# Kernel optimization log

Measured on AMD Instinct MI355X. Metric: run time of the kernel, lower is better.

Reference implementation:

```python
import jax, jax.numpy as jnp
import numpy as np

N_USERS = 100000  # n_users + 1 (padding idx)
N_ITEMS = 100000  # n_items + 1
N_NODES = N_USERS + N_ITEMS
EMBED = 64
N_BEHAVIORS = 3
N_EDGES = 2000000
BATCH = 4096
REG_WEIGHT = 1e-4


def setup_inputs() -> dict:
    key = jax.random.key(0)
    ks = jax.random.split(key, 6)
    user_emb = jax.random.normal(ks[0], (N_USERS, EMBED), dtype=jnp.float32) * 0.05
    item_emb = jax.random.normal(ks[1], (N_ITEMS, EMBED), dtype=jnp.float32) * 0.05
    gcn_weight = jax.random.normal(ks[2], (N_BEHAVIORS, EMBED, EMBED), dtype=jnp.float32) * (1.0 / np.sqrt(EMBED))
    gcn_bias = jnp.zeros((N_BEHAVIORS, EMBED), dtype=jnp.float32)
    edges = jax.random.randint(ks[3], (N_BEHAVIORS, 2, N_EDGES), 0, N_NODES, dtype=jnp.int64)
    batch_data = jax.random.randint(ks[4], (BATCH, N_BEHAVIORS, 3), 0, N_USERS, dtype=jnp.int64)
    return {"user_emb": user_emb, "item_emb": item_emb, "gcn_weight": gcn_weight,
            "gcn_bias": gcn_bias, "edges": edges, "batch_data": batch_data}


def _gcn_conv(x, row, col, W, b):
    # PyG GCNConv, add_self_loops=False: out = D^-1/2 A D^-1/2 (x W) + b
    x = x @ W  # [N, d]
    deg = jax.ops.segment_sum(jnp.ones_like(col, dtype=x.dtype), col, num_segments=N_NODES)
    dinv = jnp.where(deg > 0, jax.lax.rsqrt(jnp.maximum(deg, 1.0)) * (deg > 0), 0.0)
    norm = dinv[row] * dinv[col]  # [E]
    msg = norm[:, None] * x[row]  # [E, d] gather + scale
    out = jax.ops.segment_sum(msg, col, num_segments=N_NODES)  # scatter-add
    return out + b


def _l2_normalize(x, eps=1e-12):
    n = jnp.sqrt(jnp.sum(x * x, axis=-1, keepdims=True))
    return x / jnp.maximum(n, eps)


def reference(user_emb, item_emb, gcn_weight, gcn_bias, edges, batch_data):
    total = jnp.concatenate([user_emb, item_emb], axis=0)  # [N_NODES, d]
    total_loss = jnp.float32(0.0)
    for bi in range(N_BEHAVIORS):
        row, col = edges[bi, 0], edges[bi, 1]
        layer = _gcn_conv(total, row, col, gcn_weight[bi], gcn_bias[bi])
        layer = _l2_normalize(layer)
        total = layer + total  # residual accumulation across behaviors
        u_all, i_all = total[:N_USERS], total[N_USERS:]
        users = batch_data[:, bi, 0]          # [B]
        items = batch_data[:, bi, 1:]         # [B, 2] (pos, neg)
        u_feat = u_all[users]                 # [B, d]
        i_feat = i_all[items]                 # [B, 2, d]
        scores = jnp.einsum('bd,bkd->bk', u_feat, i_feat)  # [B, 2]
        bpr = -jnp.mean(jax.nn.log_sigmoid(scores[:, 0] - scores[:, 1]))
        total_loss = total_loss + bpr
    emb_loss = 0.5 * (jnp.sum(user_emb * user_emb) + jnp.sum(item_emb * item_emb)) / BATCH
    total_loss = total_loss + REG_WEIGHT * emb_loss
    return total_loss
```

## Files before the change

### kernel.cpp

```cpp
#include <hip/hip_runtime.h>

#define N_USERS  100000
#define N_ITEMS  100000
#define N_NODES  200000
#define EMBED    64
#define NB       3
#define N_EDGESC 2000000
#define NE_TOT   (NB * N_EDGESC)
#define BATCH    4096
#define M_SEG    (NB * N_NODES)
#define NPART    500
#define PSIZE    400
#define NBUCK    (NB * NPART)
#define NBLKB    256
#define EPB      8192
#define STAGE_CAP 4416
#define GEMM_BLOCKS 3125
#define AGG_BLOCKS 6250
#define NPARTS   (GEMM_BLOCKS + NB * 1024)

typedef unsigned short u16;
typedef __attribute__((ext_vector_type(8))) short short8;
typedef __attribute__((ext_vector_type(4))) float f32x4;

__device__ __forceinline__ float b2f(u16 h) {
    return __uint_as_float(((unsigned)h) << 16);
}
__device__ __forceinline__ u16 f2b(float f) {
    unsigned u = __float_as_uint(f);
    return (u16)((u + 0x7FFF + ((u >> 16) & 1)) >> 16);
}

__global__ __launch_bounds__(256) void scatterA(const int* __restrict__ edges,
                                                int* __restrict__ H) {
    __shared__ int h[NPART];
    int bi  = blockIdx.x / NBLKB;
    int blk = blockIdx.x - bi * NBLKB;
    const int* cols = edges + ((size_t)bi * 2 + 1) * N_EDGESC;
    for (int i = threadIdx.x; i < NPART; i += 256) h[i] = 0;
    __syncthreads();
    int base0 = blk * EPB;
#pragma unroll 4
    for (int it = 0; it < EPB / 256; ++it) {
        int idx = base0 + it * 256 + threadIdx.x;
        if (idx < N_EDGESC) atomicAdd(&h[cols[idx] / PSIZE], 1);
    }
    __syncthreads();
    for (int i = threadIdx.x; i < NPART; i += 256)
        H[(bi * NPART + i) * NBLKB + blk] = h[i];
}

__global__ __launch_bounds__(256) void colscan(int* __restrict__ H,
                                               int* __restrict__ bCnt) {
    int wid = blockIdx.x * 4 + (threadIdx.x >> 6);
    if (wid >= NBUCK) return;
    int lane = threadIdx.x & 63;
    int carry = 0;
#pragma unroll
    for (int ch = 0; ch < NBLKB / 64; ++ch) {
        int i = wid * NBLKB + ch * 64 + lane;
        int v = H[i];
        int s = v;
#pragma unroll
        for (int off = 1; off < 64; off <<= 1) {
            int tt = __shfl_up(s, off, 64);
            if (lane >= off) s += tt;
        }
        H[i] = carry + s - v;
        carry += __shfl(s, 63, 64);
    }
    if (lane == 0) bCnt[wid] = carry;
}

__global__ __launch_bounds__(256) void scan_buckets(const int* __restrict__ bCnt,
                                                    int* __restrict__ bBase,
                                                    int* __restrict__ startv) {
    __shared__ int s[NBUCK + 1];
    __shared__ int tsum[256];
    int t = threadIdx.x;
    const int IT = (NBUCK + 255) / 256;
    int base0 = t * IT;
    int vals[IT];
    int sum = 0;
#pragma unroll
    for (int k = 0; k < IT; ++k) {
        int i = base0 + k;
        vals[k] = (i < NBUCK) ? bCnt[i] : 0;
        sum += vals[k];
    }
    tsum[t] = sum;
    __syncthreads();
    for (int off = 1; off < 256; off <<= 1) {
        int v = (t >= off) ? tsum[t - off] : 0;
        __syncthreads();
        tsum[t] += v;
        __syncthreads();
    }
    int run = tsum[t] - sum;
#pragma unroll
    for (int k = 0; k < IT; ++k) {
        int i = base0 + k;
        if (i < NBUCK) s[i] = run;
        run += vals[k];
    }
    if (t == 255) {
        s[NBUCK] = run;
        startv[M_SEG] = run;
    }
    __syncthreads();
    for (int i = t; i < NBUCK + 1; i += 256) bBase[i] = s[i];
}

__global__ __launch_bounds__(256) void scatterB(const int* __restrict__ edges,
                                                const int* __restrict__ H,
                                                const int* __restrict__ bCnt,
                                                const int* __restrict__ bBase,
                                                int* __restrict__ bpack) {
    __shared__ int cur[NPART + 2];
    __shared__ int lstart[NPART + 1];
    __shared__ int sbase[NPART];
    __shared__ int tsum[256];
    __shared__ int stage[EPB];
    int bi  = blockIdx.x / NBLKB;
    int blk = blockIdx.x - bi * NBLKB;
    const int* rows = edges + ((size_t)bi * 2 + 0) * N_EDGESC;
    const int* cols = edges + ((size_t)bi * 2 + 1) * N_EDGESC;
    int t = threadIdx.x;

    for (int i = t; i < NPART; i += 256) {
        int b  = bi * NPART + i;
        int hc = H[b * NBLKB + blk];
        int nx = (blk < NBLKB - 1) ? H[b * NBLKB + blk + 1] : bCnt[b];
        sbase[i] = bBase[b] + hc;
        cur[i]   = nx - hc;
    }
    if (t == 0) cur[NPART] = 0;
    __syncthreads();

    int sb0 = t * 2;
    int v0 = (sb0     <= NPART) ? cur[sb0]     : 0;
    int v1 = (sb0 + 1 <= NPART) ? cur[sb0 + 1] : 0;
    int sum = v0 + v1;
    tsum[t] = sum;
    __syncthreads();
    for (int off = 1; off < 256; off <<= 1) {
        int v = (t >= off) ? tsum[t - off] : 0;
        __syncthreads();
        tsum[t] += v;
        __syncthreads();
    }
    int run = tsum[t] - sum;
    __syncthreads();
    if (sb0     <= NPART) { cur[sb0]     = run;      lstart[sb0]     = run; }
    if (sb0 + 1 <= NPART) { cur[sb0 + 1] = run + v0; lstart[sb0 + 1] = run + v0; }
    __syncthreads();

    int base0 = blk * EPB;
    for (int it = 0; it < EPB / 256; it += 4) {
        int i0 = base0 + (it + 0) * 256 + t;
        int i1 = base0 + (it + 1) * 256 + t;
        int i2 = base0 + (it + 2) * 256 + t;
        int i3 = base0 + (it + 3) * 256 + t;
        int c0 = (i0 < N_EDGESC) ? cols[i0] : -1;
        int c1 = (i1 < N_EDGESC) ? cols[i1] : -1;
        int c2 = (i2 < N_EDGESC) ? cols[i2] : -1;
        int c3 = (i3 < N_EDGESC) ? cols[i3] : -1;
        int r0 = (i0 < N_EDGESC) ? rows[i0] : 0;
        int r1 = (i1 < N_EDGESC) ? rows[i1] : 0;
        int r2 = (i2 < N_EDGESC) ? rows[i2] : 0;
        int r3 = (i3 < N_EDGESC) ? rows[i3] : 0;
        if (c0 >= 0) { int p = c0 / PSIZE; int q = atomicAdd(&cur[p], 1);
                       stage[q] = ((c0 - p * PSIZE) << 18) | r0; }
        if (c1 >= 0) { int p = c1 / PSIZE; int q = atomicAdd(&cur[p], 1);
                       stage[q] = ((c1 - p * PSIZE) << 18) | r1; }
        if (c2 >= 0) { int p = c2 / PSIZE; int q = atomicAdd(&cur[p], 1);
                       stage[q] = ((c2 - p * PSIZE) << 18) | r2; }
        if (c3 >= 0) { int p = c3 / PSIZE; int q = atomicAdd(&cur[p], 1);
                       stage[q] = ((c3 - p * PSIZE) << 18) | r3; }
    }
    __syncthreads();

    int grp = t >> 4;
    int li  = t & 15;
    for (int p = grp; p < NPART; p += 16) {
        int lb  = lstart[p];
        int len = lstart[p + 1] - lb;
        int gb  = sbase[p];
        for (int off = li; off < len; off += 16)
            bpack[gb + off] = stage[lb + off];
    }
}

__global__ __launch_bounds__(256) void place_kernel(const int* __restrict__ bpack,
                                                    const int* __restrict__ bBase,
                                                    int* __restrict__ startv,
                                                    float* __restrict__ dinv,
                                                    int* __restrict__ srow) {
    __shared__ int cnt[PSIZE + 2];
    __shared__ int tsum[256];
    __shared__ int stage[STAGE_CAP];
    int b    = blockIdx.x;
    int bi   = b / NPART;
    int part = b - bi * NPART;
    int segBase = bi * N_NODES + part * PSIZE;
    int lo = bBase[b], hiEnd = bBase[b + 1];
    int t = threadIdx.x;

    for (int i = t; i < PSIZE + 1; i += 256) cnt[i] = 0;
    __syncthreads();

    {
        int i = lo + t;
        for (; i + 768 < hiEnd; i += 1024) {
            int a0 = bpack[i];
            int a1 = bpack[i + 256];
            int a2 = bpack[i + 512];
            int a3 = bpack[i + 768];
            atomicAdd(&cnt[a0 >> 18], 1);
            atomicAdd(&cnt[a1 >> 18], 1);
            atomicAdd(&cnt[a2 >> 18], 1);
            atomicAdd(&cnt[a3 >> 18], 1);
        }
        for (; i < hiEnd; i += 256) atomicAdd(&cnt[bpack[i] >> 18], 1);
    }
    __syncthreads();

    int base0 = t * 2;
    int v0 = (base0     <= PSIZE) ? cnt[base0]     : 0;
    int v1 = (base0 + 1 <= PSIZE) ? cnt[base0 + 1] : 0;
    int sum = v0 + v1;
    tsum[t] = sum;
    __syncthreads();
    for (int off = 1; off < 256; off <<= 1) {
        int v = (t >= off) ? tsum[t - off] : 0;
        __syncthreads();
        tsum[t] += v;
        __syncthreads();
    }
    int run = tsum[t] - sum;
    __syncthreads();
    if (base0     <= PSIZE) cnt[base0]     = run;
    if (base0 + 1 <= PSIZE) cnt[base0 + 1] = run + v0;
    __syncthreads();

    for (int i = t; i < PSIZE; i += 256) {
        int excl = cnt[i];
        int d    = cnt[i + 1] - excl;
        startv[segBase + i] = lo + excl;
        dinv[segBase + i]   = (d > 0) ? rsqrtf((float)d) : 0.0f;
    }
    __syncthreads();

    {
        int i = lo + t;
        for (; i + 768 < hiEnd; i += 1024) {
            int p0 = bpack[i];
            int p1 = bpack[i + 256];
            int p2 = bpack[i + 512];
            int p3 = bpack[i + 768];
            int q0 = atomicAdd(&cnt[p0 >> 18], 1);
            int q1 = atomicAdd(&cnt[p1 >> 18], 1);
            int q2 = atomicAdd(&cnt[p2 >> 18], 1);
            int q3 = atomicAdd(&cnt[p3 >> 18], 1);
            if (q0 < STAGE_CAP) stage[q0] = p0 & 0x3FFFF; else srow[lo + q0] = p0 & 0x3FFFF;
            if (q1 < STAGE_CAP) stage[q1] = p1 & 0x3FFFF; else srow[lo + q1] = p1 & 0x3FFFF;
            if (q2 < STAGE_CAP) stage[q2] = p2 & 0x3FFFF; else srow[lo + q2] = p2 & 0x3FFFF;
            if (q3 < STAGE_CAP) stage[q3] = p3 & 0x3FFFF; else srow[lo + q3] = p3 & 0x3FFFF;
        }
        for (; i < hiEnd; i += 256) {
            int pk  = bpack[i];
            int pos = atomicAdd(&cnt[pk >> 18], 1);
            if (pos < STAGE_CAP) stage[pos] = pk & 0x3FFFF; else srow[lo + pos] = pk & 0x3FFFF;
        }
    }
    __syncthreads();

    int n = hiEnd - lo;
    int cap = (n < STAGE_CAP) ? n : STAGE_CAP;
    for (int i = t; i < cap; i += 256) srow[lo + i] = stage[i];
}

__device__ __forceinline__ void load_Bfrag(const float* __restrict__ W,
                                           int lane, short8 Bf[4][2]) {
    int n    = lane & 15;
    int kb   = (lane >> 4) * 8;
#pragma unroll
    for (int ct = 0; ct < 4; ++ct)
#pragma unroll
        for (int kt = 0; kt < 2; ++kt)
#pragma unroll
            for (int j = 0; j < 8; ++j)
                Bf[ct][kt][j] = (short)f2b(W[(kt * 32 + kb + j) * 64 + ct * 16 + n]);
}

__device__ __forceinline__ void store_tile(u16* __restrict__ x16,
                                           const float* __restrict__ dinv, int base,
                                           int r0, int lane, const f32x4 acc[4]) {
    int col  = lane & 15;
    int rowb = (lane >> 4) * 4;
    float dv[4];
#pragma unroll
    for (int j = 0; j < 4; ++j) dv[j] = dinv[base + r0 + rowb + j];
#pragma unroll
    for (int ct = 0; ct < 4; ++ct)
#pragma unroll
        for (int j = 0; j < 4; ++j)
            x16[(size_t)(r0 + rowb + j) * 64 + ct * 16 + col] = f2b(acc[ct][j] * dv[j]);
}

__global__ __launch_bounds__(256) void mfma_first(const float* __restrict__ ue,
                                                  const float* __restrict__ ie,
                                                  const float* __restrict__ W,
                                                  const float* __restrict__ dinv,
                                                  u16* __restrict__ x16,
                                                  float* __restrict__ regpart) {
    __shared__ float wsum[4];
    int lane = threadIdx.x & 63;
    short8 Bf[4][2];
    load_Bfrag(W, lane, Bf);

    int r0 = (blockIdx.x * 4 + (threadIdx.x >> 6)) * 16;
    int m  = lane & 15;
    int kb = (lane >> 4) * 8;
    int r  = r0 + m;
    const float* src = (r < N_USERS) ? (ue + (size_t)r * 64)
                                     : (ie + (size_t)(r - N_USERS) * 64);
    float sq = 0.0f;
    short8 A0, A1;
#pragma unroll
    for (int h = 0; h < 2; ++h) {
        float4 a = ((const float4*)(src + h * 32 + kb))[0];
        float4 b = ((const float4*)(src + h * 32 + kb))[1];
        short8& A = h ? A1 : A0;
        A[0] = (short)f2b(a.x); A[1] = (short)f2b(a.y);
        A[2] = (short)f2b(a.z); A[3] = (short)f2b(a.w);
        A[4] = (short)f2b(b.x); A[5] = (short)f2b(b.y);
        A[6] = (short)f2b(b.z); A[7] = (short)f2b(b.w);
        sq += a.x * a.x + a.y * a.y + a.z * a.z + a.w * a.w;
        sq += b.x * b.x + b.y * b.y + b.z * b.z + b.w * b.w;
    }
    f32x4 acc[4];
#pragma unroll
    for (int ct = 0; ct < 4; ++ct) {
        acc[ct] = (f32x4){0.f, 0.f, 0.f, 0.f};
        acc[ct] = __builtin_amdgcn_mfma_f32_16x16x32_bf16(A0, Bf[ct][0], acc[ct], 0, 0, 0);
        acc[ct] = __builtin_amdgcn_mfma_f32_16x16x32_bf16(A1, Bf[ct][1], acc[ct], 0, 0, 0);
    }
    store_tile(x16, dinv, 0, r0, lane, acc);

#pragma unroll
    for (int off = 32; off; off >>= 1) sq += __shfl_xor(sq, off, 64);
    if (lane == 0) wsum[threadIdx.x >> 6] = sq;
    __syncthreads();
    if (threadIdx.x == 0)
        regpart[blockIdx.x] = (wsum[0] + wsum[1] + wsum[2] + wsum[3]) *
                              (0.5f * 0.0001f / (float)BATCH);
}

__global__ __launch_bounds__(256) void mfma_gemm(const u16* __restrict__ g16,
                                                 const float* __restrict__ W,
                                                 const float* __restrict__ dinv,
                                                 int base,
                                                 u16* __restrict__ x16) {
    int lane = threadIdx.x & 63;
    short8 Bf[4][2];
    load_Bfrag(W, lane, Bf);

    int r0 = (blockIdx.x * 4 + (threadIdx.x >> 6)) * 16;
    int m  = lane & 15;
    int kb = (lane >> 4) * 8;
    const u16* src = g16 + (size_t)(r0 + m) * 64 + kb;
    short8 A0 = *(const short8*)(src);
    short8 A1 = *(const short8*)(src + 32);
    f32x4 acc[4];
#pragma unroll
    for (int ct = 0; ct < 4; ++ct) {
        acc[ct] = (f32x4){0.f, 0.f, 0.f, 0.f};
        acc[ct] = __builtin_amdgcn_mfma_f32_16x16x32_bf16(A0, Bf[ct][0], acc[ct], 0, 0, 0);
        acc[ct] = __builtin_amdgcn_mfma_f32_16x16x32_bf16(A1, Bf[ct][1], acc[ct], 0, 0, 0);
    }
    store_tile(x16, dinv, base, r0, lane, acc);
}

__global__ __launch_bounds__(256) void agg_kernel(const int* __restrict__ srow,
                                                  const int* __restrict__ startv,
                                                  const float* __restrict__ dinv,
                                                  const int4* __restrict__ xv,
                                                  const float4* __restrict__ reslo,
                                                  const float4* __restrict__ reshi,
                                                  const int4* __restrict__ res16,
                                                  int resf32,
                                                  int4* __restrict__ g16out,
                                                  const float* __restrict__ bias,
                                                  int base ) {
    int lane = threadIdx.x & 63;
    int li   = lane & 7;
    int c = (blockIdx.x * 4 + (threadIdx.x >> 6)) * 8 + (lane >> 3);

    int   s   = startv[base + c];
    int   end = startv[base + c + 1];
    float dc  = dinv[base + c];

    float acc[8];
#pragma unroll
    for (int d = 0; d < 8; ++d) acc[d] = 0.0f;

    int e = s;
    for (; e + 8 <= end; e += 8) {
#pragma unroll
        for (int jj = 0; jj < 8; ++jj) {
            int r = srow[e + jj];
            int4 w = xv[(size_t)r * 8 + li];
            acc[0] += __uint_as_float(((unsigned)w.x) << 16);
            acc[1] += __uint_as_float(((unsigned)w.x) & 0xFFFF0000u);
            acc[2] += __uint_as_float(((unsigned)w.y) << 16);
            acc[3] += __uint_as_float(((unsigned)w.y) & 0xFFFF0000u);
            acc[4] += __uint_as_float(((unsigned)w.z) << 16);
            acc[5] += __uint_as_float(((unsigned)w.z) & 0xFFFF0000u);
            acc[6] += __uint_as_float(((unsigned)w.w) << 16);
            acc[7] += __uint_as_float(((unsigned)w.w) & 0xFFFF0000u);
        }
    }
    if (e < end) {
#pragma unroll
        for (int jj = 0; jj < 8; ++jj) {
            int  ej = e + jj;
            bool ok = ej < end;
            int  ec = ok ? ej : s;
            int  r  = srow[ec];
            int4 w  = xv[(size_t)r * 8 + li];
            float m = ok ? 1.0f : 0.0f;
            acc[0] += m * __uint_as_float(((unsigned)w.x) << 16);
            acc[1] += m * __uint_as_float(((unsigned)w.x) & 0xFFFF0000u);
            acc[2] += m * __uint_as_float(((unsigned)w.y) << 16);
            acc[3] += m * __uint_as_float(((unsigned)w.y) & 0xFFFF0000u);
            acc[4] += m * __uint_as_float(((unsigned)w.z) << 16);
            acc[5] += m * __uint_as_float(((unsigned)w.z) & 0xFFFF0000u);
            acc[6] += m * __uint_as_float(((unsigned)w.w) << 16);
            acc[7] += m * __uint_as_float(((unsigned)w.w) & 0xFFFF0000u);
        }
    }

    float4 b0 = ((const float4*)bias)[li * 2];
    float4 b1 = ((const float4*)bias)[li * 2 + 1];
    float v[8];
    v[0] = acc[0] * dc + b0.x; v[1] = acc[1] * dc + b0.y;
    v[2] = acc[2] * dc + b0.z; v[3] = acc[3] * dc + b0.w;
    v[4] = acc[4] * dc + b1.x; v[5] = acc[5] * dc + b1.y;
    v[6] = acc[6] * dc + b1.z; v[7] = acc[7] * dc + b1.w;
    float sq = 0.0f;
#pragma unroll
    for (int d = 0; d < 8; ++d) sq += v[d] * v[d];
    sq += __shfl_xor(sq, 1, 64);
    sq += __shfl_xor(sq, 2, 64);
    sq += __shfl_xor(sq, 4, 64);
    float inv = 1.0f / fmaxf(sqrtf(sq), 1e-12f);

    float rv[8];
    if (resf32) {
        const float4* rsrc = (c < N_USERS)
            ? reslo + ((size_t)c * 16 + li * 2)
            : reshi + ((size_t)(c - N_USERS) * 16 + li * 2);
        float4 t0 = rsrc[0], t1 = rsrc[1];
        rv[0] = t0.x; rv[1] = t0.y; rv[2] = t0.z; rv[3] = t0.w;
        rv[4] = t1.x; rv[5] = t1.y; rv[6] = t1.z; rv[7] = t1.w;
    } else {
        int4 rw = res16[(size_t)c * 8 + li];
        rv[0] = __uint_as_float(((unsigned)rw.x) << 16);
        rv[1] = __uint_as_float(((unsigned)rw.x) & 0xFFFF0000u);
        rv[2] = __uint_as_float(((unsigned)rw.y) << 16);
        rv[3] = __uint_as_float(((unsigned)rw.y) & 0xFFFF0000u);
        rv[4] = __uint_as_float(((unsigned)rw.z) << 16);
        rv[5] = __uint_as_float(((unsigned)rw.z) & 0xFFFF0000u);
        rv[6] = __uint_as_float(((unsigned)rw.w) << 16);
        rv[7] = __uint_as_float(((unsigned)rw.w) & 0xFFFF0000u);
    }
    float o[8];
#pragma unroll
    for (int d = 0; d < 8; ++d) o[d] = rv[d] + v[d] * inv;
    int4 h;
    h.x = (int)(((unsigned)f2b(o[0])) | (((unsigned)f2b(o[1])) << 16));
    h.y = (int)(((unsigned)f2b(o[2])) | (((unsigned)f2b(o[3])) << 16));
    h.z = (int)(((unsigned)f2b(o[4])) | (((unsigned)f2b(o[5])) << 16));
    h.w = (int)(((unsigned)f2b(o[6])) | (((unsigned)f2b(o[7])) << 16));
    g16out[(size_t)c * 8 + li] = h;
}

__global__ __launch_bounds__(256) void bpr_kernel(const u16* __restrict__ g16,
                                                  const int* __restrict__ batch,
                                                  int bi, float* __restrict__ bprpart) {
    __shared__ float sp4[4];
    int b    = blockIdx.x * 4 + (threadIdx.x >> 6);
    int lane = threadIdx.x & 63;
    int u  = batch[((size_t)b * NB + bi) * 3 + 0];
    int i0 = batch[((size_t)b * NB + bi) * 3 + 1];
    int i1 = batch[((size_t)b * NB + bi) * 3 + 2];
    float uf = b2f(g16[(size_t)u * 64 + lane]);
    float f0 = b2f(g16[(size_t)(N_USERS + i0) * 64 + lane]);
    float f1 = b2f(g16[(size_t)(N_USERS + i1) * 64 + lane]);
    float d  = uf * (f0 - f1);
#pragma unroll
    for (int off = 32; off; off >>= 1) d += __shfl_xor(d, off, 64);
    float sp = (d > 0.0f) ? log1pf(expf(-d)) : (-d + log1pf(expf(d)));
    if (lane == 0) sp4[threadIdx.x >> 6] = sp;
    __syncthreads();
    if (threadIdx.x == 0)
        bprpart[blockIdx.x] = (sp4[0] + sp4[1] + sp4[2] + sp4[3]) * (1.0f / BATCH);
}

__global__ __launch_bounds__(256) void final_write(const float* __restrict__ parts,
                                                   float* __restrict__ out) {
    __shared__ float ws[4];
    float s = 0.0f;
    for (int i = threadIdx.x; i < NPARTS; i += 256) s += parts[i];
#pragma unroll
    for (int off = 32; off; off >>= 1) s += __shfl_xor(s, off, 64);
    if ((threadIdx.x & 63) == 0) ws[threadIdx.x >> 6] = s;
    __syncthreads();
    if (threadIdx.x == 0) out[0] = ws[0] + ws[1] + ws[2] + ws[3];
}

extern "C" void kernel_launch(void* const* d_in, const int* in_sizes, int n_in,
                              void* d_out, int out_size, void* d_ws, size_t ws_size,
                              hipStream_t stream) {
    const float* user_emb = (const float*)d_in[0];
    const float* item_emb = (const float*)d_in[1];
    const float* gcn_w    = (const float*)d_in[2];
    const float* gcn_b    = (const float*)d_in[3];
    const int*   edges    = (const int*)d_in[4];
    const int*   batch    = (const int*)d_in[5];
    float*       out      = (float*)d_out;

    const size_t NODE_F = (size_t)N_NODES * EMBED;
    u16*     g16A   = (u16*)d_ws;
    u16*     g16B   = g16A + NODE_F;
    u16*     x16    = g16B + NODE_F;
    float*   dinv   = (float*)(x16 + NODE_F);
    int*     startv = (int*)(dinv + M_SEG);
    int*     Hglob  = startv + M_SEG + 1;
    int*     bCnt   = Hglob + NBUCK * NBLKB;
    int*     bBase  = bCnt + NBUCK;
    int*     bpack  = bBase + NBUCK + 1;
    int*     srow   = bpack + NE_TOT;
    float*   parts  = (float*)(srow + NE_TOT);
    float*   regpart = parts;
    float*   bprpart = parts + GEMM_BLOCKS;

    scatterA<<<NB * NBLKB, 256, 0, stream>>>(edges, Hglob);
    colscan<<<(NBUCK + 3) / 4, 256, 0, stream>>>(Hglob, bCnt);
    scan_buckets<<<1, 256, 0, stream>>>(bCnt, bBase, startv);
    scatterB<<<NB * NBLKB, 256, 0, stream>>>(edges, Hglob, bCnt, bBase, bpack);
    place_kernel<<<NBUCK, 256, 0, stream>>>(bpack, bBase, startv, dinv, srow);

    mfma_first<<<GEMM_BLOCKS, 256, 0, stream>>>(user_emb, item_emb,
                                                gcn_w, dinv, x16, regpart);

    agg_kernel<<<AGG_BLOCKS, 256, 0, stream>>>(
        srow, startv, dinv, (const int4*)x16,
        (const float4*)user_emb, (const float4*)item_emb,
        (const int4*)0, 1,
        (int4*)g16A, gcn_b, 0);
    bpr_kernel<<<1024, 256, 0, stream>>>(g16A, batch, 0, bprpart);

    u16* gcur = g16A;
    u16* gnxt = g16B;
    for (int bi = 1; bi < NB; ++bi) {
        mfma_gemm<<<GEMM_BLOCKS, 256, 0, stream>>>(
            gcur, gcn_w + (size_t)bi * EMBED * EMBED, dinv, bi * N_NODES, x16);
        agg_kernel<<<AGG_BLOCKS, 256, 0, stream>>>(
            srow, startv, dinv, (const int4*)x16,
            (const float4*)0, (const float4*)0,
            (const int4*)gcur, 0,
            (int4*)gnxt, gcn_b + bi * EMBED, bi * N_NODES);
        bpr_kernel<<<1024, 256, 0, stream>>>(gnxt, batch, bi, bprpart + bi * 1024);
        u16* tmp = gcur; gcur = gnxt; gnxt = tmp;
    }
    final_write<<<1, 256, 0, stream>>>(parts, out);
}
```

Measured before the change: 384.1 us.

## Assign one wavefront per destination node in aggregation, splitting edges across lane groups

```diff
diff --git a/kernel.cpp b/kernel.cpp
--- a/kernel.cpp
+++ b/kernel.cpp
@@ -16,7 +16,7 @@
 #define EPB      8192
 #define STAGE_CAP 4416
 #define GEMM_BLOCKS 3125
-#define AGG_BLOCKS 6250
+#define AGG_BLOCKS 50000
 #define NPARTS   (GEMM_BLOCKS + NB * 1024)
 
 typedef unsigned short u16;
@@ -395,7 +395,8 @@
                                                   int base ) {
     int lane = threadIdx.x & 63;
     int li   = lane & 7;
-    int c = (blockIdx.x * 4 + (threadIdx.x >> 6)) * 8 + (lane >> 3);
+    int eg   = lane >> 3;
+    int c = blockIdx.x * 4 + (threadIdx.x >> 6);
 
     int   s   = startv[base + c];
     int   end = startv[base + c + 1];
@@ -405,40 +406,42 @@
 #pragma unroll
     for (int d = 0; d < 8; ++d) acc[d] = 0.0f;
 
-    int e = s;
-    for (; e + 8 <= end; e += 8) {
-#pragma unroll
-        for (int jj = 0; jj < 8; ++jj) {
-            int r = srow[e + jj];
-            int4 w = xv[(size_t)r * 8 + li];
-            acc[0] += __uint_as_float(((unsigned)w.x) << 16);
-            acc[1] += __uint_as_float(((unsigned)w.x) & 0xFFFF0000u);
-            acc[2] += __uint_as_float(((unsigned)w.y) << 16);
-            acc[3] += __uint_as_float(((unsigned)w.y) & 0xFFFF0000u);
-            acc[4] += __uint_as_float(((unsigned)w.z) << 16);
-            acc[5] += __uint_as_float(((unsigned)w.z) & 0xFFFF0000u);
-            acc[6] += __uint_as_float(((unsigned)w.w) << 16);
-            acc[7] += __uint_as_float(((unsigned)w.w) & 0xFFFF0000u);
+    for (int e = s; e < end; e += 16) {
+        int  e0 = e + eg;
+        bool k0 = e0 < end;
+        int  r0 = srow[k0 ? e0 : s];
+        int4 w0 = xv[(size_t)r0 * 8 + li];
+        float m0 = k0 ? 1.0f : 0.0f;
+        acc[0] += m0 * __uint_as_float(((unsigned)w0.x) << 16);
+        acc[1] += m0 * __uint_as_float(((unsigned)w0.x) & 0xFFFF0000u);
+        acc[2] += m0 * __uint_as_float(((unsigned)w0.y) << 16);
+        acc[3] += m0 * __uint_as_float(((unsigned)w0.y) & 0xFFFF0000u);
+        acc[4] += m0 * __uint_as_float(((unsigned)w0.z) << 16);
+        acc[5] += m0 * __uint_as_float(((unsigned)w0.z) & 0xFFFF0000u);
+        acc[6] += m0 * __uint_as_float(((unsigned)w0.w) << 16);
+        acc[7] += m0 * __uint_as_float(((unsigned)w0.w) & 0xFFFF0000u);
+        if (e + 8 < end) {
+            int  e1 = e + 8 + eg;
+            bool k1 = e1 < end;
+            int  r1 = srow[k1 ? e1 : s];
+            int4 w1 = xv[(size_t)r1 * 8 + li];
+            float m1 = k1 ? 1.0f : 0.0f;
+            acc[0] += m1 * __uint_as_float(((unsigned)w1.x) << 16);
+            acc[1] += m1 * __uint_as_float(((unsigned)w1.x) & 0xFFFF0000u);
+            acc[2] += m1 * __uint_as_float(((unsigned)w1.y) << 16);
+            acc[3] += m1 * __uint_as_float(((unsigned)w1.y) & 0xFFFF0000u);
+            acc[4] += m1 * __uint_as_float(((unsigned)w1.z) << 16);
+            acc[5] += m1 * __uint_as_float(((unsigned)w1.z) & 0xFFFF0000u);
+            acc[6] += m1 * __uint_as_float(((unsigned)w1.w) << 16);
+            acc[7] += m1 * __uint_as_float(((unsigned)w1.w) & 0xFFFF0000u);
         }
     }
-    if (e < end) {
-#pragma unroll
-        for (int jj = 0; jj < 8; ++jj) {
-            int  ej = e + jj;
-            bool ok = ej < end;
-            int  ec = ok ? ej : s;
-            int  r  = srow[ec];
-            int4 w  = xv[(size_t)r * 8 + li];
-            float m = ok ? 1.0f : 0.0f;
-            acc[0] += m * __uint_as_float(((unsigned)w.x) << 16);
-            acc[1] += m * __uint_as_float(((unsigned)w.x) & 0xFFFF0000u);
-            acc[2] += m * __uint_as_float(((unsigned)w.y) << 16);
-            acc[3] += m * __uint_as_float(((unsigned)w.y) & 0xFFFF0000u);
-            acc[4] += m * __uint_as_float(((unsigned)w.z) << 16);
-            acc[5] += m * __uint_as_float(((unsigned)w.z) & 0xFFFF0000u);
-            acc[6] += m * __uint_as_float(((unsigned)w.w) << 16);
-            acc[7] += m * __uint_as_float(((unsigned)w.w) & 0xFFFF0000u);
-        }
+
+#pragma unroll
+    for (int d = 0; d < 8; ++d) {
+        acc[d] += __shfl_xor(acc[d], 8, 64);
+        acc[d] += __shfl_xor(acc[d], 16, 64);
+        acc[d] += __shfl_xor(acc[d], 32, 64);
     }
 
     float4 b0 = ((const float4*)bias)[li * 2];
@@ -456,34 +459,36 @@
     sq += __shfl_xor(sq, 4, 64);
     float inv = 1.0f / fmaxf(sqrtf(sq), 1e-12f);
 
-    float rv[8];
-    if (resf32) {
-        const float4* rsrc = (c < N_USERS)
-            ? reslo + ((size_t)c * 16 + li * 2)
-            : reshi + ((size_t)(c - N_USERS) * 16 + li * 2);
-        float4 t0 = rsrc[0], t1 = rsrc[1];
-        rv[0] = t0.x; rv[1] = t0.y; rv[2] = t0.z; rv[3] = t0.w;
-        rv[4] = t1.x; rv[5] = t1.y; rv[6] = t1.z; rv[7] = t1.w;
-    } else {
-        int4 rw = res16[(size_t)c * 8 + li];
-        rv[0] = __uint_as_float(((unsigned)rw.x) << 16);
-        rv[1] = __uint_as_float(((unsigned)rw.x) & 0xFFFF0000u);
-        rv[2] = __uint_as_float(((unsigned)rw.y) << 16);
-        rv[3] = __uint_as_float(((unsigned)rw.y) & 0xFFFF0000u);
-        rv[4] = __uint_as_float(((unsigned)rw.z) << 16);
-        rv[5] = __uint_as_float(((unsigned)rw.z) & 0xFFFF0000u);
-        rv[6] = __uint_as_float(((unsigned)rw.w) << 16);
-        rv[7] = __uint_as_float(((unsigned)rw.w) & 0xFFFF0000u);
-    }
-    float o[8];
-#pragma unroll
-    for (int d = 0; d < 8; ++d) o[d] = rv[d] + v[d] * inv;
-    int4 h;
-    h.x = (int)(((unsigned)f2b(o[0])) | (((unsigned)f2b(o[1])) << 16));
-    h.y = (int)(((unsigned)f2b(o[2])) | (((unsigned)f2b(o[3])) << 16));
-    h.z = (int)(((unsigned)f2b(o[4])) | (((unsigned)f2b(o[5])) << 16));
-    h.w = (int)(((unsigned)f2b(o[6])) | (((unsigned)f2b(o[7])) << 16));
-    g16out[(size_t)c * 8 + li] = h;
+    if (eg == 0) {
+        float rv[8];
+        if (resf32) {
+            const float4* rsrc = (c < N_USERS)
+                ? reslo + ((size_t)c * 16 + li * 2)
+                : reshi + ((size_t)(c - N_USERS) * 16 + li * 2);
+            float4 t0 = rsrc[0], t1 = rsrc[1];
+            rv[0] = t0.x; rv[1] = t0.y; rv[2] = t0.z; rv[3] = t0.w;
+            rv[4] = t1.x; rv[5] = t1.y; rv[6] = t1.z; rv[7] = t1.w;
+        } else {
+            int4 rw = res16[(size_t)c * 8 + li];
+            rv[0] = __uint_as_float(((unsigned)rw.x) << 16);
+            rv[1] = __uint_as_float(((unsigned)rw.x) & 0xFFFF0000u);
+            rv[2] = __uint_as_float(((unsigned)rw.y) << 16);
+            rv[3] = __uint_as_float(((unsigned)rw.y) & 0xFFFF0000u);
+            rv[4] = __uint_as_float(((unsigned)rw.z) << 16);
+            rv[5] = __uint_as_float(((unsigned)rw.z) & 0xFFFF0000u);
+            rv[6] = __uint_as_float(((unsigned)rw.w) << 16);
+            rv[7] = __uint_as_float(((unsigned)rw.w) & 0xFFFF0000u);
+        }
+        float o[8];
+#pragma unroll
+        for (int d = 0; d < 8; ++d) o[d] = rv[d] + v[d] * inv;
+        int4 h;
+        h.x = (int)(((unsigned)f2b(o[0])) | (((unsigned)f2b(o[1])) << 16));
+        h.y = (int)(((unsigned)f2b(o[2])) | (((unsigned)f2b(o[3])) << 16));
+        h.z = (int)(((unsigned)f2b(o[4])) | (((unsigned)f2b(o[5])) << 16));
+        h.w = (int)(((unsigned)f2b(o[6])) | (((unsigned)f2b(o[7])) << 16));
+        g16out[(size_t)c * 8 + li] = h;
+    }
 }
 
 __global__ __launch_bounds__(256) void bpr_kernel(const u16* __restrict__ g16,
```

After: 502.6 us. 30.8% more time.
